# Kernel tuning notes

Hardware: AMD Instinct MI355X
Metric: run time of the kernel (lower is better)

Reference implementation:

```python
import jax, jax.numpy as jnp
import numpy as np

EPS = 1e-09
K = 16


def setup_inputs() -> dict:
    key = jax.random.key(0)
    ks = jax.random.split(key, 20)
    B, N, D, E, T = 1024, 100000, 64, 64, 8
    s = 0.02
    inp = {
        "x": jax.random.normal(ks[0], (B, D), jnp.float32),
        "memory_inputs": jax.random.normal(ks[1], (N, D), jnp.float32),
        "memory_targets": jax.random.normal(ks[2], (N, T), jnp.float32),
        # local encoder: D -> E -> E
        "le_w1": s * jax.random.normal(ks[3], (D, E), jnp.float32),
        "le_b1": jnp.zeros((E,), jnp.float32),
        "le_w2": s * jax.random.normal(ks[4], (E, E), jnp.float32),
        "le_b2": jnp.zeros((E,), jnp.float32),
        "feature_weights": 0.1 * jnp.ones((E,), jnp.float32),
        "inv_temp": jnp.float32(1.0),
        # global encoder: D -> 128 -> 64 -> 64
        "ge_w1": s * jax.random.normal(ks[5], (D, 128), jnp.float32),
        "ge_b1": jnp.zeros((128,), jnp.float32),
        "ge_w2": s * jax.random.normal(ks[6], (128, 64), jnp.float32),
        "ge_b2": jnp.zeros((64,), jnp.float32),
        "ge_w3": s * jax.random.normal(ks[7], (64, 64), jnp.float32),
        "ge_b3": jnp.zeros((64,), jnp.float32),
        "gr_w1": s * jax.random.normal(ks[8], (64, 64), jnp.float32),
        "gr_b1": jnp.zeros((64,), jnp.float32),
        "gr_w2": s * jax.random.normal(ks[9], (64, T), jnp.float32),
        "gr_b2": jnp.zeros((T,), jnp.float32),
        # gate: (64+E) -> 64 -> 1
        "gate_w1": s * jax.random.normal(ks[10], (64 + E, 64), jnp.float32),
        "gate_b1": jnp.zeros((64,), jnp.float32),
        "gate_w2": s * jax.random.normal(ks[11], (64, 1), jnp.float32),
        "gate_b2": jnp.zeros((1,), jnp.float32),
        # refinement: T -> max(32,4T)=32 -> T
        "rh_w1": s * jax.random.normal(ks[12], (T, 32), jnp.float32),
        "rh_b1": jnp.zeros((32,), jnp.float32),
        "rh_w2": s * jax.random.normal(ks[13], (32, T), jnp.float32),
        "rh_b2": jnp.zeros((T,), jnp.float32),
    }
    return inp


def _mlp2(x, w1, b1, w2, b2):
    return jax.nn.relu(x @ w1 + b1) @ w2 + b2


def reference(x, memory_inputs, memory_targets,
              le_w1, le_b1, le_w2, le_b2,
              feature_weights, inv_temp,
              ge_w1, ge_b1, ge_w2, ge_b2, ge_w3, ge_b3,
              gr_w1, gr_b1, gr_w2, gr_b2,
              gate_w1, gate_b1, gate_w2, gate_b2,
              rh_w1, rh_b1, rh_w2, rh_b2):
    # local embeddings for queries and memory
    q_emb = _mlp2(x, le_w1, le_b1, le_w2, le_b2)                 # (B, E)
    mem_emb = _mlp2(memory_inputs, le_w1, le_b1, le_w2, le_b2)   # (N, E)

    # weighted squared euclidean distances (cdist(...)^2 expansion)
    sqrt_w = jnp.sqrt(jax.nn.softplus(feature_weights) + EPS)    # (E,)
    qw = q_emb * sqrt_w                                          # (B, E)
    mw = mem_emb * sqrt_w                                        # (N, E)
    d2 = (jnp.sum(qw * qw, axis=1)[:, None]
          + jnp.sum(mw * mw, axis=1)[None, :]
          - 2.0 * (qw @ mw.T))                                   # (B, N)
    d2 = jnp.maximum(d2, 0.0)

    temp = jax.nn.softplus(inv_temp) + EPS
    raw_acts = jnp.exp(-d2 / (temp + EPS))                        # (B, N)

    # top-k select + softmax over selected activations (eval mode: no dropout)
    topk_vals, topk_idx = jax.lax.top_k(raw_acts, K)              # (B, K)
    topk_weights = jax.nn.softmax(topk_vals, axis=1)              # (B, K)

    neigh_targets = memory_targets[topk_idx]                      # (B, K, T)
    local_pred = jnp.einsum('bk,bkt->bt', topk_weights, neigh_targets)  # (B, T)

    # global path: D -> 128 -> 64 -> 64 (ReLU after each hidden)
    h = jax.nn.relu(x @ ge_w1 + ge_b1)
    h = jax.nn.relu(h @ ge_w2 + ge_b2)
    global_repr = h @ ge_w3 + ge_b3                               # (B, 64)
    global_pred = _mlp2(global_repr, gr_w1, gr_b1, gr_w2, gr_b2)  # (B, T)

    # gate in [0, 1]
    gate_in = jnp.concatenate([global_repr, q_emb], axis=1)       # (B, 64+E)
    g = jax.nn.sigmoid(jax.nn.relu(gate_in @ gate_w1 + gate_b1) @ gate_w2 + gate_b2)  # (B, 1)

    blended = g * local_pred + (1.0 - g) * global_pred            # (B, T)
    out = _mlp2(blended, rh_w1, rh_b1, rh_w2, rh_b2)              # (B, T)
    return out
```

## Files before the change

### kernel.cpp

```cpp
#include <hip/hip_runtime.h>
#include <math.h>

#define N_MEM 100000
#define NP    100352
#define JBLK  1024
#define NJB   98
#define QCAP  1024
#define NCAND 128

__device__ __forceinline__ float softplusf_(float x){ return log1pf(expf(x)); }

__device__ __forceinline__ double wave_sum_d(double v){
  #pragma unroll
  for (int o=32;o;o>>=1) v += __shfl_xor(v, o, 64);
  return v;
}
__device__ __forceinline__ int wave_sum_i(int v){
  #pragma unroll
  for (int o=32;o;o>>=1) v += __shfl_xor(v, o, 64);
  return v;
}

__device__ __forceinline__ void wave_argmax3(float& v, int& j, int& p){
  #pragma unroll
  for (int o=32;o;o>>=1){
    float ov = __shfl_xor(v, o, 64);
    int   oj = __shfl_xor(j, o, 64);
    int   op = __shfl_xor(p, o, 64);
    if (ov > v || (ov == v && oj < j)) { v = ov; j = oj; p = op; }
  }
}

__device__ __forceinline__ float bitonic_sort64(float v, int lane){
  #pragma unroll
  for (int k=2;k<=64;k<<=1){
    #pragma unroll
    for (int j=k>>1;j>0;j>>=1){
      float o = __shfl_xor(v, j, 64);
      float mn = fminf(v,o), mx = fmaxf(v,o);
      bool upper = (lane & j) != 0;
      bool asc   = ((lane & k) == 0);
      v = (upper == asc) ? mx : mn;
    }
  }
  return v;
}

#define SCORE_LOOP_16x4_SQ() { \
  _Pragma("unroll 4") \
  for (int d=0; d<64; d++){ \
    float4 mv4 = *(const float4*)(rowbase + (size_t)d*NP); \
    float marr[4]={mv4.x,mv4.y,mv4.z,mv4.w}; \
    _Pragma("unroll") \
    for (int qi_=0;qi_<16;qi_++){ \
      float qv_ = qbase[qi_*64 + d]; \
      _Pragma("unroll") \
      for (int jj_=0;jj_<4;jj_++) s[qi_][jj_] = fmaf(qv_, marr[jj_], s[qi_][jj_]); \
    } \
  } }

__global__ __launch_bounds__(128) void k1_mem(
    const float* __restrict__ mi,
    const float* __restrict__ w1, const float* __restrict__ b1,
    const float* __restrict__ w2, const float* __restrict__ b2,
    const float* __restrict__ fw,
    float* __restrict__ mwT, float* __restrict__ mm)
{
  __shared__ float xs[64*128];
  int t = threadIdx.x;
  int j = blockIdx.x*128 + t;
  bool real = (j < N_MEM);
  {
    const float4* xp = (const float4*)(mi + (size_t)(real ? j : 0)*64);
    #pragma unroll
    for (int k=0;k<16;k++){
      float4 v = xp[k];
      xs[(4*k+0)*128 + t] = v.x;
      xs[(4*k+1)*128 + t] = v.y;
      xs[(4*k+2)*128 + t] = v.z;
      xs[(4*k+3)*128 + t] = v.w;
    }
  }
  float h[64];
  #pragma unroll
  for (int e=0;e<64;e++) h[e] = b1[e];
  for (int d=0; d<64; d++){
    float xv = xs[d*128 + t];
    #pragma unroll
    for (int e=0;e<64;e++) h[e] = fmaf(xv, w1[d*64+e], h[e]);
  }
  #pragma unroll
  for (int e=0;e<64;e++){ h[e] = fmaxf(h[e], 0.f); xs[e*128 + t] = h[e]; }
  float o[64];
  #pragma unroll
  for (int e=0;e<64;e++) o[e] = b2[e];
  for (int d=0; d<64; d++){
    float hv = xs[d*128 + t];
    #pragma unroll
    for (int e=0;e<64;e++) o[e] = fmaf(hv, w2[d*64+e], o[e]);
  }
  float s2 = 0.f;
  #pragma unroll
  for (int e=0;e<64;e++){
    float sw = sqrtf(softplusf_(fw[e]) + 1e-9f);
    float v = real ? o[e]*sw : 0.f;
    s2 = fmaf(v, v, s2);
    mwT[(size_t)e*NP + j] = v;
  }
  mm[j] = real ? s2 : 3.0e38f;
}

__global__ __launch_bounds__(64) void k2_query(
  const float* __restrict__ x,
  const float* __restrict__ le_w1, const float* __restrict__ le_b1,
  const float* __restrict__ le_w2, const float* __restrict__ le_b2,
  const float* __restrict__ fw,
  const float* __restrict__ ge_w1, const float* __restrict__ ge_b1,
  const float* __restrict__ ge_w2, const float* __restrict__ ge_b2,
  const float* __restrict__ ge_w3, const float* __restrict__ ge_b3,
  const float* __restrict__ gr_w1, const float* __restrict__ gr_b1,
  const float* __restrict__ gr_w2, const float* __restrict__ gr_b2,
  const float* __restrict__ ga_w1, const float* __restrict__ ga_b1,
  const float* __restrict__ ga_w2, const float* __restrict__ ga_b2,
  float* __restrict__ qwf, double* __restrict__ qwd,
  double* __restrict__ qqd, double* __restrict__ ggd, double* __restrict__ gpd,
  int* __restrict__ qcnt)
{
  int l = threadIdx.x, q = blockIdx.x;
  if (l==0) qcnt[q] = 0;
  __shared__ double xs[64], qe[64], h1[128], t1[64], t2[64];
  xs[l] = (double)x[q*64+l];
  __syncthreads();
  double a0,a1,a2,a3,a;
  a0=a1=a2=a3=0.0;
  for (int d=0; d<64; d+=4){
    a0 = fma(xs[d  ], (double)le_w1[(d  )*64+l], a0);
    a1 = fma(xs[d+1], (double)le_w1[(d+1)*64+l], a1);
    a2 = fma(xs[d+2], (double)le_w1[(d+2)*64+l], a2);
    a3 = fma(xs[d+3], (double)le_w1[(d+3)*64+l], a3);
  }
  a = ((a0+a1)+(a2+a3)) + (double)le_b1[l];
  t1[l] = a > 0.0 ? a : 0.0;
  __syncthreads();
  a0=a1=a2=a3=0.0;
  for (int d=0; d<64; d+=4){
    a0 = fma(t1[d  ], (double)le_w2[(d  )*64+l], a0);
    a1 = fma(t1[d+1], (double)le_w2[(d+1)*64+l], a1);
    a2 = fma(t1[d+2], (double)le_w2[(d+2)*64+l], a2);
    a3 = fma(t1[d+3], (double)le_w2[(d+3)*64+l], a3);
  }
  a = ((a0+a1)+(a2+a3)) + (double)le_b2[l];
  qe[l] = a;
  double sw = sqrt(log1p(exp((double)fw[l])) + 1e-9);
  double qv = a * sw;
  qwd[q*64+l] = qv;
  qwf[q*64+l] = (float)qv;
  double ss = wave_sum_d(qv*qv);
  if (l==0) qqd[q] = ss;
  double b0=0,b1v=0,c0=0,c1=0;
  for (int d=0; d<64; d+=2){
    double x0 = xs[d], x1 = xs[d+1];
    b0  = fma(x0, (double)ge_w1[(d  )*128+l],    b0);
    b1v = fma(x1, (double)ge_w1[(d+1)*128+l],    b1v);
    c0  = fma(x0, (double)ge_w1[(d  )*128+64+l], c0);
    c1  = fma(x1, (double)ge_w1[(d+1)*128+64+l], c1);
  }
  a = (b0+b1v) + (double)ge_b1[l];
  double c = (c0+c1) + (double)ge_b1[64+l];
  h1[l] = a>0.0?a:0.0; h1[64+l] = c>0.0?c:0.0;
  __syncthreads();
  a0=a1=a2=a3=0.0;
  for (int d=0; d<128; d+=4){
    a0 = fma(h1[d  ], (double)ge_w2[(d  )*64+l], a0);
    a1 = fma(h1[d+1], (double)ge_w2[(d+1)*64+l], a1);
    a2 = fma(h1[d+2], (double)ge_w2[(d+2)*64+l], a2);
    a3 = fma(h1[d+3], (double)ge_w2[(d+3)*64+l], a3);
  }
  a = ((a0+a1)+(a2+a3)) + (double)ge_b2[l];
  __syncthreads();
  t1[l] = a>0.0?a:0.0;
  __syncthreads();
  a0=a1=a2=a3=0.0;
  for (int d=0; d<64; d+=4){
    a0 = fma(t1[d  ], (double)ge_w3[(d  )*64+l], a0);
    a1 = fma(t1[d+1], (double)ge_w3[(d+1)*64+l], a1);
    a2 = fma(t1[d+2], (double)ge_w3[(d+2)*64+l], a2);
    a3 = fma(t1[d+3], (double)ge_w3[(d+3)*64+l], a3);
  }
  a = ((a0+a1)+(a2+a3)) + (double)ge_b3[l];
  t2[l] = a;
  __syncthreads();
  a0=a1=a2=a3=0.0;
  for (int d=0; d<64; d+=4){
    a0 = fma(t2[d  ], (double)gr_w1[(d  )*64+l], a0);
    a1 = fma(t2[d+1], (double)gr_w1[(d+1)*64+l], a1);
    a2 = fma(t2[d+2], (double)gr_w1[(d+2)*64+l], a2);
    a3 = fma(t2[d+3], (double)gr_w1[(d+3)*64+l], a3);
  }
  a = ((a0+a1)+(a2+a3)) + (double)gr_b1[l];
  __syncthreads();
  t1[l] = a>0.0?a:0.0;
  __syncthreads();
  if (l < 8){
    a0=a1=a2=a3=0.0;
    for (int d=0; d<64; d+=4){
      a0 = fma(t1[d  ], (double)gr_w2[(d  )*8+l], a0);
      a1 = fma(t1[d+1], (double)gr_w2[(d+1)*8+l], a1);
      a2 = fma(t1[d+2], (double)gr_w2[(d+2)*8+l], a2);
      a3 = fma(t1[d+3], (double)gr_w2[(d+3)*8+l], a3);
    }
    gpd[q*8+l] = ((a0+a1)+(a2+a3)) + (double)gr_b2[l];
  }
  a0=a1=a2=a3=0.0;
  for (int d=0; d<64; d+=4){
    a0 = fma(t2[d  ], (double)ga_w1[(d  )*64+l], a0);
    a1 = fma(t2[d+1], (double)ga_w1[(d+1)*64+l], a1);
    a2 = fma(t2[d+2], (double)ga_w1[(d+2)*64+l], a2);
    a3 = fma(t2[d+3], (double)ga_w1[(d+3)*64+l], a3);
  }
  for (int d=0; d<64; d+=4){
    a0 = fma(qe[d  ], (double)ga_w1[(64+d  )*64+l], a0);
    a1 = fma(qe[d+1], (double)ga_w1[(64+d+1)*64+l], a1);
    a2 = fma(qe[d+2], (double)ga_w1[(64+d+2)*64+l], a2);
    a3 = fma(qe[d+3], (double)ga_w1[(64+d+3)*64+l], a3);
  }
  a = ((a0+a1)+(a2+a3)) + (double)ga_b1[l];
  a = a>0.0?a:0.0;
  double p = wave_sum_d(a * (double)ga_w2[l]);
  if (l==0) ggd[q] = 1.0/(1.0 + exp(-(p + (double)ga_b2[0])));
}

__global__ __launch_bounds__(256) void k_tau(
    const float* __restrict__ mwT, const float* __restrict__ mm,
    const float* __restrict__ qw, float* __restrict__ ssc)
{
  int t = threadIdx.x, w = t>>6, lane = t&63;
  int q0 = blockIdx.x*16;
  int jb = blockIdx.y*JBLK;
  const float* qbase = qw + (size_t)q0*64;
  int jw = jb + w*256 + 4*lane;
  const float* rowbase = mwT + jw;
  float s[16][4];
  #pragma unroll
  for (int a=0;a<16;a++){
    #pragma unroll
    for (int b=0;b<4;b++) s[a][b]=0.f;
  }
  SCORE_LOOP_16x4_SQ();
  float4 mmv4 = *(const float4*)(mm + jw);
  float mmv[4] = {mmv4.x, mmv4.y, mmv4.z, mmv4.w};
  #pragma unroll
  for (int qi=0;qi<16;qi++){
    int qg = q0 + qi;
    float4 o0;
    o0.x = 2.f*s[qi][0]-mmv[0]; o0.y = 2.f*s[qi][1]-mmv[1];
    o0.z = 2.f*s[qi][2]-mmv[2]; o0.w = 2.f*s[qi][3]-mmv[3];
    *(float4*)(ssc + (size_t)qg*4096 + jw) = o0;
  }
}

__global__ __launch_bounds__(256) void k_tau_sel(
    const float* __restrict__ ssc, float* __restrict__ tau)
{
  int t = threadIdx.x, w = t>>6, l = t&63, q = blockIdx.x;
  __shared__ unsigned su[4096];
  __shared__ int rs[4];
  const float* base = ssc + (size_t)q*4096;
  for (int i=t; i<4096; i+=256){
    unsigned f = __float_as_uint(base[i]);
    su[i] = f ^ ((f >> 31) ? 0xFFFFFFFFu : 0x80000000u);
  }
  __syncthreads();
  unsigned T = 0u;
  for (int b=31; b>=0; b--){
    unsigned cand = T | (1u<<b);
    int c = 0;
    for (int i=t; i<4096; i+=256) c += (su[i] >= cand) ? 1 : 0;
    c = wave_sum_i(c);
    if (l==0) rs[w] = c;
    __syncthreads();
    int tot = rs[0]+rs[1]+rs[2]+rs[3];
    if (tot >= 16) T = cand;
    __syncthreads();
  }
  if (t==0){
    unsigned f = (T & 0x80000000u) ? (T ^ 0x80000000u) : ~T;
    tau[q] = __uint_as_float(f);
  }
}

__global__ __launch_bounds__(256) void k3_main(
    const float* __restrict__ mwT, const float* __restrict__ mm,
    const float* __restrict__ qw,  const float* __restrict__ tau,
    int* __restrict__ qcnt, float* __restrict__ qcv, int* __restrict__ qci)
{
  int t=threadIdx.x, w=t>>6, lane=t&63;
  int q0 = blockIdx.x*16;
  int jb = blockIdx.y*JBLK;
  __shared__ float taus[16];
  const float* qbase = qw + (size_t)q0*64;
  if (t < 16){ taus[t] = tau[q0+t] - 5e-6f; }
  __syncthreads();
  int jw = jb + w*256 + 4*lane;
  const float* rowbase = mwT + jw;
  float s[16][4];
  #pragma unroll
  for (int a=0;a<16;a++){
    #pragma unroll
    for (int b=0;b<4;b++) s[a][b]=0.f;
  }
  SCORE_LOOP_16x4_SQ();
  float4 mmv4 = *(const float4*)(mm + jw);
  float mmv[4] = {mmv4.x, mmv4.y, mmv4.z, mmv4.w};
  #pragma unroll
  for (int qi=0;qi<16;qi++){
    float tq = taus[qi];
    int qg = q0 + qi;
    #pragma unroll
    for (int jj=0;jj<4;jj++){
      float sc = 2.f*s[qi][jj] - mmv[jj];
      if (sc >= tq){
        int p = atomicAdd(&qcnt[qg], 1);
        if (p < QCAP){
          qcv[(size_t)qg*QCAP+p] = sc;
          qci[(size_t)qg*QCAP+p] = jw + jj;
        }
      }
    }
  }
}

__global__ __launch_bounds__(256) void k4_pre(
    const int* __restrict__ qcnt, const float* __restrict__ qcv, const int* __restrict__ qci,
    int* __restrict__ candjG, int* __restrict__ nc2G)
{
  int t = threadIdx.x, l = t&63, q = blockIdx.x;
  __shared__ float  svv[QCAP];
  __shared__ int    sii[QCAP];
  __shared__ float  v16s;
  __shared__ int    ncnt2;
  int NC = qcnt[q]; NC = NC < QCAP ? NC : QCAP;
  for (int i=t; i<NC; i+=256){ svv[i]=qcv[(size_t)q*QCAP+i]; sii[i]=qci[(size_t)q*QCAP+i]; }
  if (t==0) ncnt2 = 0;
  __syncthreads();
  if (t < 64){
    float vm = -3.0e38f;
    for (int i=l; i<NC; i+=64) vm = fmaxf(vm, svv[i]);
    vm = bitonic_sort64(vm, l);
    if (l == 48) v16s = vm;
  }
  __syncthreads();
  {
    float thr = v16s - 2e-6f;
    for (int i=t; i<NC; i+=256){
      if (svv[i] >= thr && (unsigned)sii[i] < (unsigned)N_MEM){
        int p = atomicAdd(&ncnt2, 1);
        if (p < NCAND) candjG[(size_t)q*NCAND + p] = sii[i];
      }
    }
  }
  __syncthreads();
  if (t==0) nc2G[q] = ncnt2 < NCAND ? ncnt2 : NCAND;
}

__global__ __launch_bounds__(256) void k4_emb(
    const int* __restrict__ candjG, const int* __restrict__ nc2G,
    const double* __restrict__ qwd_g, const double* __restrict__ qqd_g,
    const float* __restrict__ mi,
    const float* __restrict__ le_w1, const float* __restrict__ le_b1,
    const float* __restrict__ le_w2, const float* __restrict__ le_b2,
    const float* __restrict__ fw, double* __restrict__ cd2G)
{
  int t = threadIdx.x, w = t>>6, l = t&63, q = blockIdx.x;
  __shared__ float  lw1[4096], lw2[4096];
  __shared__ double hdw[4][64];
  for (int i=t; i<4096; i+=256){ lw1[i]=le_w1[i]; lw2[i]=le_w2[i]; }
  __syncthreads();
  int NC2 = nc2G[q];
  double qwl = qwd_g[q*64+l];
  double swl = sqrt(log1p(exp((double)fw[l])) + 1e-9);
  double qq  = qqd_g[q];
  double lb1 = (double)le_b1[l], lb2 = (double)le_b2[l];
  for (int c = blockIdx.y*4 + w; c < NC2; c += 8){
    int jc = __builtin_amdgcn_readfirstlane(candjG[(size_t)q*NCAND + c]);
    const float* mrow = mi + (size_t)jc*64;
    double b0=0,b1=0,b2=0,b3=0,b4=0,b5=0,b6=0,b7=0;
    #pragma unroll
    for (int d=0; d<64; d+=8){
      b0 = fma((double)mrow[d  ], (double)lw1[(d  )*64+l], b0);
      b1 = fma((double)mrow[d+1], (double)lw1[(d+1)*64+l], b1);
      b2 = fma((double)mrow[d+2], (double)lw1[(d+2)*64+l], b2);
      b3 = fma((double)mrow[d+3], (double)lw1[(d+3)*64+l], b3);
      b4 = fma((double)mrow[d+4], (double)lw1[(d+4)*64+l], b4);
      b5 = fma((double)mrow[d+5], (double)lw1[(d+5)*64+l], b5);
      b6 = fma((double)mrow[d+6], (double)lw1[(d+6)*64+l], b6);
      b7 = fma((double)mrow[d+7], (double)lw1[(d+7)*64+l], b7);
    }
    double h = (((b0+b1)+(b2+b3)) + ((b4+b5)+(b6+b7))) + lb1;
    h = h>0.0 ? h : 0.0;
    hdw[w][l] = h;
    double c0=0,c1=0,c2=0,c3=0,c4=0,c5=0,c6=0,c7=0;
    #pragma unroll
    for (int d=0; d<64; d+=8){
      c0 = fma(hdw[w][d  ], (double)lw2[(d  )*64+l], c0);
      c1 = fma(hdw[w][d+1], (double)lw2[(d+1)*64+l], c1);
      c2 = fma(hdw[w][d+2], (double)lw2[(d+2)*64+l], c2);
      c3 = fma(hdw[w][d+3], (double)lw2[(d+3)*64+l], c3);
      c4 = fma(hdw[w][d+4], (double)lw2[(d+4)*64+l], c4);
      c5 = fma(hdw[w][d+5], (double)lw2[(d+5)*64+l], c5);
      c6 = fma(hdw[w][d+6], (double)lw2[(d+6)*64+l], c6);
      c7 = fma(hdw[w][d+7], (double)lw2[(d+7)*64+l], c7);
    }
    double o  = (((c0+c1)+(c2+c3)) + ((c4+c5)+(c6+c7))) + lb2;
    double mw = o * swl;
    double sc = wave_sum_d(mw*(mw - 2.0*qwl));
    if (l==0) cd2G[(size_t)q*NCAND + c] = qq + sc;
  }
}

__global__ __launch_bounds__(64) void k4_fin(
    const int* __restrict__ candjG, const int* __restrict__ nc2G,
    const double* __restrict__ cd2G,
    const double* __restrict__ ggd_g, const double* __restrict__ gpd_g,
    const float* __restrict__ mt, const float* __restrict__ itp,
    const float* __restrict__ rw1, const float* __restrict__ rb1,
    const float* __restrict__ rw2, const float* __restrict__ rb2,
    float* __restrict__ out)
{
  int l = threadIdx.x, q = blockIdx.x;
  __shared__ float  selr[16];
  __shared__ int    selj[16];
  __shared__ double hh[32];
  int NC2 = nc2G[q];
  {
    float e32  = (float)exp((double)itp[0]);
    float sp32 = (float)log1p((double)e32);
    float t32  = __fadd_rn(sp32, 1e-9f);
    float dn32 = __fadd_rn(t32, 1e-9f);
    double denom = (double)dn32;
    float r0=-2.f, r1=-2.f; int j0=0x7fffffff, j1=0x7fffffff;
    if (l < NC2){
      double d2 = cd2G[(size_t)q*NCAND + l]; if (d2 < 0.0) d2 = 0.0;
      float ratio32 = (float)(d2 / denom);
      r0 = (float)exp(-(double)ratio32);
      j0 = candjG[(size_t)q*NCAND + l];
    }
    if (l+64 < NC2){
      double d2 = cd2G[(size_t)q*NCAND + l+64]; if (d2 < 0.0) d2 = 0.0;
      float ratio32 = (float)(d2 / denom);
      r1 = (float)exp(-(double)ratio32);
      j1 = candjG[(size_t)q*NCAND + l+64];
    }
    bool u0=false, u1=false;
    for (int it=0; it<16; it++){
      float a0 = u0 ? -2.f : r0;
      float a1 = u1 ? -2.f : r1;
      float v; int j; int p;
      if (a0 > a1 || (a0 == a1 && j0 <= j1)) { v=a0; j=j0; p=l*2; }
      else                                   { v=a1; j=j1; p=l*2+1; }
      wave_argmax3(v, j, p);
      if ((p>>1) == l){ if (p&1) u1=true; else u0=true; }
      if (l == it){ selr[it]=v; selj[it]=j; }
    }
  }
  __syncthreads();
  double raw = (l<16) ? (double)selr[l] : -1.0e300;
  double mv = raw;
  #pragma unroll
  for (int o=32;o;o>>=1){ double ov = __shfl_xor(mv,o,64); mv = ov>mv?ov:mv; }
  double e  = (l<16) ? exp(raw - mv) : 0.0;
  double se = wave_sum_d(e);
  double wgt = e / se;
  double lp[8] = {0,0,0,0,0,0,0,0};
  if (l < 16){
    const float* tr = mt + (size_t)selj[l]*8;
    #pragma unroll
    for (int tt=0; tt<8; tt++) lp[tt] = wgt * (double)tr[tt];
  }
  #pragma unroll
  for (int tt=0; tt<8; tt++) lp[tt] = wave_sum_d(lp[tt]);
  double g = ggd_g[q];
  double bl[8];
  #pragma unroll
  for (int tt=0; tt<8; tt++) bl[tt] = g*lp[tt] + (1.0-g)*gpd_g[q*8+tt];
  if (l < 32){
    double a = (double)rb1[l];
    #pragma unroll
    for (int tt=0; tt<8; tt++) a = fma(bl[tt], (double)rw1[tt*32+l], a);
    hh[l] = a>0.0?a:0.0;
  }
  __syncthreads();
  if (l < 8){
    double a = (double)rb2[l];
    #pragma unroll
    for (int i=0; i<32; i++) a = fma(hh[i], (double)rw2[i*8+l], a);
    out[q*8+l] = (float)a;
  }
}

extern "C" void kernel_launch(void* const* d_in, const int* in_sizes, int n_in,
                              void* d_out, int out_size, void* d_ws, size_t ws_size,
                              hipStream_t stream)
{
  const float* x     = (const float*)d_in[0];
  const float* mi    = (const float*)d_in[1];
  const float* mt    = (const float*)d_in[2];
  const float* le_w1 = (const float*)d_in[3];
  const float* le_b1 = (const float*)d_in[4];
  const float* le_w2 = (const float*)d_in[5];
  const float* le_b2 = (const float*)d_in[6];
  const float* fw    = (const float*)d_in[7];
  const float* itp   = (const float*)d_in[8];
  const float* ge_w1 = (const float*)d_in[9];
  const float* ge_b1 = (const float*)d_in[10];
  const float* ge_w2 = (const float*)d_in[11];
  const float* ge_b2 = (const float*)d_in[12];
  const float* ge_w3 = (const float*)d_in[13];
  const float* ge_b3 = (const float*)d_in[14];
  const float* gr_w1 = (const float*)d_in[15];
  const float* gr_b1 = (const float*)d_in[16];
  const float* gr_w2 = (const float*)d_in[17];
  const float* gr_b2 = (const float*)d_in[18];
  const float* ga_w1 = (const float*)d_in[19];
  const float* ga_b1 = (const float*)d_in[20];
  const float* ga_w2 = (const float*)d_in[21];
  const float* ga_b2 = (const float*)d_in[22];
  const float* rh_w1 = (const float*)d_in[23];
  const float* rh_b1 = (const float*)d_in[24];
  const float* rh_w2 = (const float*)d_in[25];
  const float* rh_b2 = (const float*)d_in[26];

  double* dws = (double*)d_ws;
  double* qwd = dws;
  double* qqd = qwd + (size_t)1024*64;
  double* ggd = qqd + 1024;
  double* gpd = ggd + 1024;
  double* cd2G= gpd + 8192;
  float*  fws = (float*)(cd2G + (size_t)1024*128);
  float* mwT = fws;
  float* mm  = mwT + (size_t)64*NP;
  float* qwf = mm  + NP;
  float* tau = qwf + (size_t)1024*64;
  float* ssc = tau + 1024;
  int*   qcnt= (int*)(ssc + (size_t)1024*4096);
  float* qcv = (float*)(qcnt + 1024);
  int*   qci = (int*)(qcv + (size_t)1024*QCAP);
  int*   candjG = qci + (size_t)1024*QCAP;
  int*   nc2G   = candjG + (size_t)1024*NCAND;

  k1_mem    <<<dim3(NP/128), dim3(128), 0, stream>>>(mi, le_w1, le_b1, le_w2, le_b2, fw, mwT, mm);
  k2_query  <<<dim3(1024),   dim3(64),  0, stream>>>(x, le_w1, le_b1, le_w2, le_b2, fw,
                ge_w1, ge_b1, ge_w2, ge_b2, ge_w3, ge_b3,
                gr_w1, gr_b1, gr_w2, gr_b2,
                ga_w1, ga_b1, ga_w2, ga_b2,
                qwf, qwd, qqd, ggd, gpd, qcnt);
  k_tau     <<<dim3(64,4),   dim3(256), 0, stream>>>(mwT, mm, qwf, ssc);
  k_tau_sel <<<dim3(1024),   dim3(256), 0, stream>>>(ssc, tau);
  k3_main   <<<dim3(64,NJB), dim3(256), 0, stream>>>(mwT, mm, qwf, tau, qcnt, qcv, qci);
  k4_pre    <<<dim3(1024),   dim3(256), 0, stream>>>(qcnt, qcv, qci, candjG, nc2G);
  k4_emb    <<<dim3(1024,2), dim3(256), 0, stream>>>(candjG, nc2G, qwd, qqd, mi,
                le_w1, le_b1, le_w2, le_b2, fw, cd2G);
  k4_fin    <<<dim3(1024),   dim3(64),  0, stream>>>(candjG, nc2G, cd2G, ggd, gpd, mt, itp,
                rh_w1, rh_b1, rh_w2, rh_b2, (float*)d_out);
}
```

Before: 517.9 us.

## Split memory encoder work across four waves by output feature slice

Memory-encoder kernel k1_mem now uses 256 threads per 128 memory rows. Each wave computes 16 output features for two rows instead of one thread holding all 64 hidden and 64 output accumulators. This cuts per-thread register pressure to raise occupancy, and the weight loads become wave-uniform. Rows are loaded cooperatively into padded shared memory, and the squared norm is reduced across waves through shared memory. The cost is extra barriers and a shared-memory round trip.

```diff
diff --git a/kernel.cpp b/kernel.cpp
--- a/kernel.cpp
+++ b/kernel.cpp
@@ -59,55 +59,85 @@
     } \
   } }
 
-__global__ __launch_bounds__(128) void k1_mem(
+__global__ __launch_bounds__(256) void k1_mem(
     const float* __restrict__ mi,
     const float* __restrict__ w1, const float* __restrict__ b1,
     const float* __restrict__ w2, const float* __restrict__ b2,
     const float* __restrict__ fw,
     float* __restrict__ mwT, float* __restrict__ mm)
 {
-  __shared__ float xs[64*128];
-  int t = threadIdx.x;
-  int j = blockIdx.x*128 + t;
-  bool real = (j < N_MEM);
+  __shared__ float xs[64*132];
+  __shared__ float mms[4][132];
+  int t = threadIdx.x, w = t>>6, lane = t&63;
+  int jb = blockIdx.x*128;
   {
-    const float4* xp = (const float4*)(mi + (size_t)(real ? j : 0)*64);
-    #pragma unroll
-    for (int k=0;k<16;k++){
+    int jl = t & 127; int j = jb + jl; int d0 = (t>>7)*32;
+    bool real = (j < N_MEM);
+    const float4* xp = (const float4*)(mi + (size_t)(real?j:0)*64 + d0);
+    #pragma unroll
+    for (int k=0;k<8;k++){
       float4 v = xp[k];
-      xs[(4*k+0)*128 + t] = v.x;
-      xs[(4*k+1)*128 + t] = v.y;
-      xs[(4*k+2)*128 + t] = v.z;
-      xs[(4*k+3)*128 + t] = v.w;
-    }
-  }
-  float h[64];
-  #pragma unroll
-  for (int e=0;e<64;e++) h[e] = b1[e];
+      if (!real){ v.x=0.f; v.y=0.f; v.z=0.f; v.w=0.f; }
+      xs[(d0+4*k+0)*132 + jl] = v.x;
+      xs[(d0+4*k+1)*132 + jl] = v.y;
+      xs[(d0+4*k+2)*132 + jl] = v.z;
+      xs[(d0+4*k+3)*132 + jl] = v.w;
+    }
+  }
+  __syncthreads();
+  int e0 = w*16;
+  int jc = 2*lane;
+  float s[16][2];
+  #pragma unroll
+  for (int qi=0;qi<16;qi++){ float b = b1[e0+qi]; s[qi][0]=b; s[qi][1]=b; }
   for (int d=0; d<64; d++){
-    float xv = xs[d*128 + t];
-    #pragma unroll
-    for (int e=0;e<64;e++) h[e] = fmaf(xv, w1[d*64+e], h[e]);
-  }
-  #pragma unroll
-  for (int e=0;e<64;e++){ h[e] = fmaxf(h[e], 0.f); xs[e*128 + t] = h[e]; }
-  float o[64];
-  #pragma unroll
-  for (int e=0;e<64;e++) o[e] = b2[e];
+    float x0 = xs[d*132 + jc], x1 = xs[d*132 + jc+1];
+    #pragma unroll
+    for (int qi=0;qi<16;qi++){
+      float wv = w1[d*64 + e0 + qi];
+      s[qi][0] = fmaf(x0, wv, s[qi][0]);
+      s[qi][1] = fmaf(x1, wv, s[qi][1]);
+    }
+  }
+  __syncthreads();
+  #pragma unroll
+  for (int qi=0;qi<16;qi++){
+    xs[(e0+qi)*132 + jc]   = fmaxf(s[qi][0], 0.f);
+    xs[(e0+qi)*132 + jc+1] = fmaxf(s[qi][1], 0.f);
+  }
+  __syncthreads();
+  #pragma unroll
+  for (int qi=0;qi<16;qi++){ float b = b2[e0+qi]; s[qi][0]=b; s[qi][1]=b; }
   for (int d=0; d<64; d++){
-    float hv = xs[d*128 + t];
-    #pragma unroll
-    for (int e=0;e<64;e++) o[e] = fmaf(hv, w2[d*64+e], o[e]);
-  }
-  float s2 = 0.f;
-  #pragma unroll
-  for (int e=0;e<64;e++){
+    float x0 = xs[d*132 + jc], x1 = xs[d*132 + jc+1];
+    #pragma unroll
+    for (int qi=0;qi<16;qi++){
+      float wv = w2[d*64 + e0 + qi];
+      s[qi][0] = fmaf(x0, wv, s[qi][0]);
+      s[qi][1] = fmaf(x1, wv, s[qi][1]);
+    }
+  }
+  int j0g = jb + jc;
+  bool r0 = (j0g < N_MEM), r1 = (j0g+1 < N_MEM);
+  float p0 = 0.f, p1 = 0.f;
+  #pragma unroll
+  for (int qi=0;qi<16;qi++){
+    int e = e0 + qi;
     float sw = sqrtf(softplusf_(fw[e]) + 1e-9f);
-    float v = real ? o[e]*sw : 0.f;
-    s2 = fmaf(v, v, s2);
-    mwT[(size_t)e*NP + j] = v;
-  }
-  mm[j] = real ? s2 : 3.0e38f;
+    float v0 = r0 ? s[qi][0]*sw : 0.f;
+    float v1 = r1 ? s[qi][1]*sw : 0.f;
+    p0 = fmaf(v0,v0,p0);
+    p1 = fmaf(v1,v1,p1);
+    float2 o2; o2.x = v0; o2.y = v1;
+    *(float2*)(mwT + (size_t)e*NP + j0g) = o2;
+  }
+  mms[w][jc] = p0; mms[w][jc+1] = p1;
+  __syncthreads();
+  if (t < 128){
+    int j = jb + t;
+    float v = ((mms[0][t] + mms[1][t]) + mms[2][t]) + mms[3][t];
+    mm[j] = (j < N_MEM) ? v : 3.0e38f;
+  }
 }
 
 __global__ __launch_bounds__(64) void k2_query(
@@ -548,7 +578,7 @@
   int*   candjG = qci + (size_t)1024*QCAP;
   int*   nc2G   = candjG + (size_t)1024*NCAND;
 
-  k1_mem    <<<dim3(NP/128), dim3(128), 0, stream>>>(mi, le_w1, le_b1, le_w2, le_b2, fw, mwT, mm);
+  k1_mem    <<<dim3(NP/128), dim3(256), 0, stream>>>(mi, le_w1, le_b1, le_w2, le_b2, fw, mwT, mm);
   k2_query  <<<dim3(1024),   dim3(64),  0, stream>>>(x, le_w1, le_b1, le_w2, le_b2, fw,
                 ge_w1, ge_b1, ge_w2, ge_b2, ge_w3, ge_b3,
                 gr_w1, gr_b1, gr_w2, gr_b2,
```

Measured after the change: 469.4 us. -9.4%, faster.
